# Optimization experiments

Hardware: AMD Instinct MI355X
Metric: run time of the kernel (lower is better)

Reference implementation:

```python
import jax, jax.numpy as jnp
import numpy as np

B, Hh, Ww, C = 16, 56, 56, 384
HEADS, WS, SHIFT = 12, 7, 3
N = WS * WS            # 49 tokens per window
NW = (Hh // WS) * (Ww // WS)  # 64 windows
HID = int(C * 4.0)
SCALE = (C // HEADS) ** -0.5
EPS = 1e-5


def _relative_position_index():
    coords = np.stack(np.meshgrid(np.arange(WS), np.arange(WS), indexing='ij')).reshape(2, -1)
    rel = (coords[:, :, None] - coords[:, None, :]).transpose(1, 2, 0)  # (N,N,2)
    rel[..., 0] += WS - 1
    rel[..., 1] += WS - 1
    rel[..., 0] *= 2 * WS - 1
    return jnp.asarray(rel.sum(-1))  # (N,N) int

RPI = _relative_position_index()


def _swin_mask():
    img = np.zeros((Hh, Ww), np.float32)
    slices = (slice(0, -WS), slice(-WS, -SHIFT), slice(-SHIFT, None))
    cnt = 0
    for hs in slices:
        for ws in slices:
            img[hs, ws] = cnt
            cnt += 1
    m = img.reshape(Hh // WS, WS, Ww // WS, WS).transpose(0, 2, 1, 3).reshape(-1, N)  # (nW,N)
    am = m[:, None, :] - m[:, :, None]
    return jnp.asarray(np.where(am != 0, -100.0, 0.0).astype(np.float32))  # (nW,N,N)


def setup_inputs() -> dict:
    key = jax.random.key(0)
    ks = jax.random.split(key, 12)
    p = lambda k, shp, s=0.02: (jax.random.normal(k, shp, jnp.float32) * s)
    return {
        'x': jax.random.normal(ks[0], (B, Hh * Ww, C), jnp.float32),
        'mask_matrix': _swin_mask(),
        'norm1_g': jnp.ones((C,), jnp.float32),
        'norm1_b': jnp.zeros((C,), jnp.float32),
        'qkv_w': p(ks[1], (3 * C, C)),
        'qkv_b': jnp.zeros((3 * C,), jnp.float32),
        'rpb_table': p(ks[2], ((2 * WS - 1) * (2 * WS - 1), HEADS)),
        'proj_w': p(ks[3], (C, C)),
        'proj_b': jnp.zeros((C,), jnp.float32),
        'norm2_g': jnp.ones((C,), jnp.float32),
        'norm2_b': jnp.zeros((C,), jnp.float32),
        'fc1_w': p(ks[4], (HID, C)),
        'fc1_b': jnp.zeros((HID,), jnp.float32),
        'fc2_w': p(ks[5], (C, HID)),
        'fc2_b': jnp.zeros((C,), jnp.float32),
    }


def _ln(x, g, b):
    m = jnp.mean(x, -1, keepdims=True)
    v = jnp.mean(jnp.square(x - m), -1, keepdims=True)
    return (x - m) * jax.lax.rsqrt(v + EPS) * g + b


def reference(x, mask_matrix, norm1_g, norm1_b, qkv_w, qkv_b, rpb_table,
              proj_w, proj_b, norm2_g, norm2_b, fc1_w, fc1_b, fc2_w, fc2_b):
    shortcut = x
    h = _ln(x, norm1_g, norm1_b).reshape(B, Hh, Ww, C)
    # cyclic shift (H,W divisible by window -> no pad)
    h = jnp.roll(h, (-SHIFT, -SHIFT), axis=(1, 2))
    # window partition -> (B*nW, N, C)
    win = h.reshape(B, Hh // WS, WS, Ww // WS, WS, C).transpose(0, 1, 3, 2, 4, 5).reshape(-1, N, C)
    B_ = win.shape[0]
    hd = C // HEADS
    qkv = (win @ qkv_w.T + qkv_b).reshape(B_, N, 3, HEADS, hd).transpose(2, 0, 3, 1, 4)
    q, k, v = qkv[0] * SCALE, qkv[1], qkv[2]  # (B_,H,N,hd)
    attn = jnp.einsum('bhnd,bhmd->bhnm', q, k)  # (B_,H,N,N)
    bias = rpb_table[RPI]  # (N,N,heads)
    attn = attn + bias.transpose(2, 0, 1)[None]
    attn = attn.reshape(B, NW, HEADS, N, N) + mask_matrix[None, :, None]
    attn = jax.nn.softmax(attn.reshape(B_, HEADS, N, N), axis=-1)
    out = jnp.einsum('bhnm,bhmd->bhnd', attn, v).transpose(0, 2, 1, 3).reshape(B_, N, C)
    out = out @ proj_w.T + proj_b
    # window reverse + reverse shift
    out = out.reshape(B, Hh // WS, Ww // WS, WS, WS, C).transpose(0, 1, 3, 2, 4, 5).reshape(B, Hh, Ww, C)
    out = jnp.roll(out, (SHIFT, SHIFT), axis=(1, 2)).reshape(B, Hh * Ww, C)
    x = shortcut + out
    h2 = _ln(x, norm2_g, norm2_b)
    h2 = jax.nn.gelu(h2 @ fc1_w.T + fc1_b, approximate=False)  # torch nn.GELU exact
    return x + (h2 @ fc2_w.T + fc2_b)
```

## Files before the change

### kernel.cpp

```cpp
#include <hip/hip_runtime.h>

typedef unsigned short u16;
typedef unsigned int u32;
typedef short s16x8 __attribute__((ext_vector_type(8)));
typedef unsigned short u16x4 __attribute__((ext_vector_type(4)));
typedef float f32x4 __attribute__((ext_vector_type(4)));

#define ATTN_SCALE 0.17677669529663687f

__device__ __forceinline__ u16 f2bf(float f) {
  union { float f; u32 i; } c; c.f = f;
  u32 r = c.i + 0x7fffu + ((c.i >> 16) & 1u);
  return (u16)(r >> 16);
}
__device__ __forceinline__ float bf2f(u16 u) {
  union { u32 i; float f; } c; c.i = ((u32)u) << 16; return c.f;
}
__device__ __forceinline__ f32x4 mfma16(s16x8 a, s16x8 b, f32x4 c) {
  return __builtin_amdgcn_mfma_f32_16x16x32_bf16(a, b, c, 0, 0, 0);
}

typedef __attribute__((address_space(1))) u32 gas_u32;
typedef __attribute__((address_space(3))) u32 las_u32;
#define GLL16(gp, lp) __builtin_amdgcn_global_load_lds((gas_u32*)(gp), (las_u32*)(lp), 16, 0, 0)

__device__ __forceinline__ int win_to_orig(int m) {
  int b = m / 3136, rem = m - b * 3136;
  int w = rem / 49, n = rem - w * 49;
  int wh = w >> 3, ww = w & 7;
  int i = n / 7, j = n - i * 7;
  int r = wh * 7 + i + 3; if (r >= 56) r -= 56;
  int c = ww * 7 + j + 3; if (c >= 56) c -= 56;
  return b * 3136 + r * 56 + c;
}

__global__ __launch_bounds__(256) void cvt_all_kernel(
    const float* __restrict__ qkvw, const float* __restrict__ projw,
    const float* __restrict__ fc1w, const float* __restrict__ fc2w,
    u16* __restrict__ wq, u16* __restrict__ wp,
    u16* __restrict__ w1, u16* __restrict__ w2) {
  int i = blockIdx.x * 256 + threadIdx.x;
  if (i < 442368) wq[i] = f2bf(qkvw[i]);
  else if (i < 589824) wp[i - 442368] = f2bf(projw[i - 442368]);
  else if (i < 1179648) w1[i - 589824] = f2bf(fc1w[i - 589824]);
  else if (i < 1769472) w2[i - 1179648] = f2bf(fc2w[i - 1179648]);
}

__global__ __launch_bounds__(256) void mk_tbl_kernel(
    const float* __restrict__ rpb, const float* __restrict__ maskp,
    u16* __restrict__ tbl) {
  int idx = blockIdx.x * 256 + threadIdx.x;
  int wh = idx >> 12;
  int rem = idx & 4095;
  int irow = rem >> 6;
  int lr = (rem >> 2) & 15, ni = rem & 3;
  int j = ni * 16 + lr;
  int wi = wh / 12, h = wh - wi * 12;
  float val = -1e30f;
  if (irow < 49 && j < 49) {
    int yi = irow / 7, xi = irow - yi * 7;
    int yj = j / 7, xj = j - yj * 7;
    int rpi = (yi - yj + 6) * 13 + (xi - xj + 6);
    val = rpb[rpi * 12 + h] + maskp[((size_t)wi * 49 + irow) * 49 + j];
  }
  tbl[idx] = f2bf(val);
}

template <bool PERM, bool BFIN>
__global__ __launch_bounds__(256) void ln_kernel(
    const void* __restrict__ xin, const float* __restrict__ g,
    const float* __restrict__ bb, u16* __restrict__ xo) {
  int t = blockIdx.x * 4 + (threadIdx.x >> 6);
  int l = threadIdx.x & 63;
  int src = PERM ? win_to_orig(t) : t;
  float v[6];
  if (BFIN) {
    const u16* row = (const u16*)xin + (size_t)src * 384;
#pragma unroll
    for (int k = 0; k < 6; k++) v[k] = bf2f(row[l + 64 * k]);
  } else {
    const float* row = (const float*)xin + (size_t)src * 384;
#pragma unroll
    for (int k = 0; k < 6; k++) v[k] = row[l + 64 * k];
  }
  float s = 0.f;
#pragma unroll
  for (int k = 0; k < 6; k++) s += v[k];
#pragma unroll
  for (int d = 1; d < 64; d <<= 1) s += __shfl_xor(s, d);
  float mean = s * (1.f / 384.f);
  float q = 0.f;
#pragma unroll
  for (int k = 0; k < 6; k++) { float dv = v[k] - mean; q += dv * dv; }
#pragma unroll
  for (int d = 1; d < 64; d <<= 1) q += __shfl_xor(q, d);
  float rstd = rsqrtf(q * (1.f / 384.f) + 1e-5f);
  u16* orow = xo + (size_t)t * 384;
#pragma unroll
  for (int k = 0; k < 6; k++) {
    int c = l + 64 * k;
    orow[c] = f2bf((v[k] - mean) * rstd * g[c] + bb[c]);
  }
}

template <int EPI>
__device__ __forceinline__ void gemm_epi(
    float v, size_t m, int col, int N, int dst,
    u16* __restrict__ outb, float* __restrict__ outf,
    const float* __restrict__ auxf, const u16* __restrict__ auxb) {
  if (EPI == 0) {
    outb[m * (size_t)N + col] = f2bf(v);
  } else if (EPI == 1) {
    outb[(size_t)dst * 384 + col] = f2bf(v + auxf[(size_t)dst * 384 + col]);
  } else if (EPI == 2) {
    float u = v * (0.7978845608028654f + 0.0356774081f * v * v);
    float gl = v / (1.f + __expf(-2.f * u));
    outb[m * (size_t)N + col] = f2bf(gl);
  } else {
    outf[m * (size_t)N + col] = v + bf2f(auxb[m * (size_t)N + col]);
  }
}

template <int EPI>
__global__ __launch_bounds__(256) void gemm128_kernel(
    const u16* __restrict__ A, const u16* __restrict__ W,
    const float* __restrict__ bias, u16* __restrict__ outb,
    float* __restrict__ outf, const float* __restrict__ auxf,
    const u16* __restrict__ auxb, int K, int N, int NT, int NB) {
  __shared__ __align__(16) short As[8192];
  __shared__ __align__(16) short Bs[8192];
  const int tid = threadIdx.x, wv = tid >> 6, l = tid & 63;
  const int lr = l & 15, lg = l >> 4;
  int bm, bn;
  {
    const int STS = NT << 3;
    const int body = (NB >> 3) * STS;
    int d = blockIdx.x;
    if (d < body) {
      int st = d / STS, rem = d - st * STS;
      bn = rem >> 3;
      bm = st * 8 + (rem & 7);
    } else {
      int t = d - body;
      int tq = t / NT;
      bm = (NB & ~7) + tq;
      bn = t - tq * NT;
    }
  }
  const size_t m0 = (size_t)bm * 128, n0 = (size_t)bn * 128;
  const int prow = wv * 16 + (l >> 2);
  const int ccl = (((l & 3) ^ ((l >> 3) & 3)) << 3);
  const u16* ga0 = A + (m0 + prow) * K + ccl;
  const u16* ga1 = A + (m0 + 64 + prow) * K + ccl;
  const u16* gb0 = W + (n0 + prow) * K + ccl;
  const u16* gb1 = W + (n0 + 64 + prow) * K + ccl;
  const int stoff = wv * 512;
  const int wr = wv >> 1, wc = wv & 1;
  const int sw = (lr >> 1) & 3;
  const int aoff = (wr * 64 + lr) * 32 + ((lg ^ sw) << 3);
  const int boff = (wc * 64 + lr) * 32 + ((lg ^ sw) << 3);

#define STAGE(bufo, koff)                            \
  do {                                               \
    GLL16(ga0 + (koff), As + (bufo) + stoff);        \
    GLL16(ga1 + (koff), As + (bufo) + 2048 + stoff); \
    GLL16(gb0 + (koff), Bs + (bufo) + stoff);        \
    GLL16(gb1 + (koff), Bs + (bufo) + 2048 + stoff); \
  } while (0)
#define FRAG_READS(cur)                                              \
  do {                                                               \
    const short* as = As + (cur);                                    \
    const short* bs = Bs + (cur);                                    \
    _Pragma("unroll") for (int mi = 0; mi < 4; mi++)                 \
        af[mi] = *(const s16x8*)&as[aoff + mi * 512];                \
    _Pragma("unroll") for (int ni = 0; ni < 4; ni++)                 \
        bfr[ni] = *(const s16x8*)&bs[boff + ni * 512];               \
  } while (0)
#define MFMA_TILE()                                        \
  do {                                                     \
    _Pragma("unroll") for (int mi = 0; mi < 4; mi++)       \
        _Pragma("unroll") for (int ni = 0; ni < 4; ni++)   \
            acc[mi][ni] = mfma16(af[mi], bfr[ni], acc[mi][ni]); \
  } while (0)

  f32x4 acc[4][4] = {};
  s16x8 af[4], bfr[4];
  STAGE(0, 0);
  STAGE(4096, 32);
  int cur = 0;
  int k0 = 0;
  for (; k0 < K - 32; k0 += 32) {
    asm volatile("s_waitcnt vmcnt(4)" ::: "memory");
    __builtin_amdgcn_sched_barrier(0);
    __builtin_amdgcn_s_barrier();
    FRAG_READS(cur);
    asm volatile("s_waitcnt lgkmcnt(0)" ::: "memory");
    __builtin_amdgcn_sched_barrier(0);
    __builtin_amdgcn_s_barrier();
    if (k0 + 64 < K) STAGE(cur, k0 + 64);
    MFMA_TILE();
    cur ^= 4096;
  }
  asm volatile("s_waitcnt vmcnt(0)" ::: "memory");
  __builtin_amdgcn_sched_barrier(0);
  __builtin_amdgcn_s_barrier();
  FRAG_READS(cur);
  asm volatile("s_waitcnt lgkmcnt(0)" ::: "memory");
  __builtin_amdgcn_sched_barrier(0);
  MFMA_TILE();
#undef STAGE
#undef FRAG_READS
#undef MFMA_TILE

  const int colb = (int)n0 + wc * 64;
#pragma unroll
  for (int mi = 0; mi < 4; mi++) {
#pragma unroll
    for (int r = 0; r < 4; r++) {
      const size_t m = m0 + wr * 64 + mi * 16 + lg * 4 + r;
      int dst = 0;
      if (EPI == 1) dst = win_to_orig((int)m);
#pragma unroll
      for (int ni = 0; ni < 4; ni++) {
        const int col = colb + ni * 16 + lr;
        gemm_epi<EPI>(acc[mi][ni][r] + bias[col], m, col, N, dst,
                      outb, outf, auxf, auxb);
      }
    }
  }
}

template <int EPI>
__global__ __launch_bounds__(512) void gemm256_kernel(
    const u16* __restrict__ A, const u16* __restrict__ W,
    const float* __restrict__ bias, u16* __restrict__ outb,
    float* __restrict__ outf, const float* __restrict__ auxf,
    const u16* __restrict__ auxb, int K, int N, int NT, int NB) {
  __shared__ __align__(16) short As[16384];
  __shared__ __align__(16) short Bs[8192];
  const int tid = threadIdx.x, wv = tid >> 6, l = tid & 63;
  const int lr = l & 15, lg = l >> 4;
  int bm, bn;
  {
    const int STS = NT << 3;
    const int body = (NB >> 3) * STS;
    int d = blockIdx.x;
    if (d < body) {
      int st = d / STS, rem = d - st * STS;
      bn = rem >> 3;
      bm = st * 8 + (rem & 7);
    } else {
      int t = d - body;
      int tq = t / NT;
      bm = (NB & ~7) + tq;
      bn = t - tq * NT;
    }
  }
  const size_t m0 = (size_t)bm * 256, n0 = (size_t)bn * 128;
  const int prow = wv * 16 + (l >> 2);
  const int ccl = (((l & 3) ^ ((l >> 3) & 3)) << 3);
  const u16* ga0 = A + (m0 + prow) * K + ccl;
  const u16* ga1 = A + (m0 + 128 + prow) * K + ccl;
  const u16* gb0 = W + (n0 + prow) * K + ccl;
  const int stoff = wv * 512;
  const int wr = wv >> 2, wc = wv & 3;
  const int sw = (lr >> 1) & 3;
  const int aoff = (wr * 128 + lr) * 32 + ((lg ^ sw) << 3);
  const int boff = (wc * 32 + lr) * 32 + ((lg ^ sw) << 3);

#define STAGE(c, koff)                                     \
  do {                                                     \
    GLL16(ga0 + (koff), As + (c) * 8192 + stoff);          \
    GLL16(ga1 + (koff), As + (c) * 8192 + 4096 + stoff);   \
    GLL16(gb0 + (koff), Bs + (c) * 4096 + stoff);          \
  } while (0)
#define FRAG_READS(c)                                                \
  do {                                                               \
    const short* as = As + (c) * 8192;                               \
    const short* bs = Bs + (c) * 4096;                               \
    _Pragma("unroll") for (int mi = 0; mi < 8; mi++)                 \
        af[mi] = *(const s16x8*)&as[aoff + mi * 512];                \
    _Pragma("unroll") for (int ni = 0; ni < 2; ni++)                 \
        bfr[ni] = *(const s16x8*)&bs[boff + ni * 512];               \
  } while (0)
#define MFMA_TILE()                                        \
  do {                                                     \
    __builtin_amdgcn_s_setprio(1);                         \
    _Pragma("unroll") for (int mi = 0; mi < 8; mi++)       \
        _Pragma("unroll") for (int ni = 0; ni < 2; ni++)   \
            acc[mi][ni] = mfma16(af[mi], bfr[ni], acc[mi][ni]); \
    __builtin_amdgcn_s_setprio(0);                         \
  } while (0)

  f32x4 acc[8][2] = {};
  s16x8 af[8], bfr[2];
  STAGE(0, 0);
  STAGE(1, 32);
  int cur = 0;
  int k0 = 0;
  for (; k0 < K - 32; k0 += 32) {
    asm volatile("s_waitcnt vmcnt(3)" ::: "memory");
    __builtin_amdgcn_sched_barrier(0);
    __builtin_amdgcn_s_barrier();
    FRAG_READS(cur);
    asm volatile("s_waitcnt lgkmcnt(0)" ::: "memory");
    __builtin_amdgcn_sched_barrier(0);
    __builtin_amdgcn_s_barrier();
    if (k0 + 64 < K) STAGE(cur, k0 + 64);
    MFMA_TILE();
    cur ^= 1;
  }
  asm volatile("s_waitcnt vmcnt(0)" ::: "memory");
  __builtin_amdgcn_sched_barrier(0);
  __builtin_amdgcn_s_barrier();
  FRAG_READS(cur);
  asm volatile("s_waitcnt lgkmcnt(0)" ::: "memory");
  __builtin_amdgcn_sched_barrier(0);
  MFMA_TILE();
#undef STAGE
#undef FRAG_READS
#undef MFMA_TILE

  const int colb = (int)n0 + wc * 32;
#pragma unroll
  for (int mi = 0; mi < 8; mi++) {
#pragma unroll
    for (int r = 0; r < 4; r++) {
      const size_t m = m0 + wr * 128 + mi * 16 + lg * 4 + r;
      int dst = 0;
      if (EPI == 1) dst = win_to_orig((int)m);
#pragma unroll
      for (int ni = 0; ni < 2; ni++) {
        const int col = colb + ni * 16 + lr;
        gemm_epi<EPI>(acc[mi][ni][r] + bias[col], m, col, N, dst,
                      outb, outf, auxf, auxb);
      }
    }
  }
}

__global__ __launch_bounds__(256) void attn_kernel(
    const u16* __restrict__ qkv, const u16* __restrict__ tbl,
    u16* __restrict__ out) {
  __shared__ __align__(16) short Pl[4][16 * 76];
  const int tid = threadIdx.x, wv = tid >> 6, l = tid & 63;
  const int lr = l & 15, lg = l >> 4;

  const int task = blockIdx.x * 4 + wv;
  const int win = task / 12, h = task - win * 12;
  const int wi = win & 63;
  const short* base = (const short*)qkv + (size_t)win * 49 * 1152 + h * 32;
  const u16* tb = tbl + (size_t)(wi * 12 + h) * 4096 + lr * 4;

  s16x8 qf[4], kf[4];
  const s16x8 zz = {0, 0, 0, 0, 0, 0, 0, 0};
#pragma unroll
  for (int mi = 0; mi < 4; mi++) {
    int n = mi * 16 + lr;
    if (n < 49) {
      qf[mi] = *(const s16x8*)(base + (size_t)n * 1152 + lg * 8);
      kf[mi] = *(const s16x8*)(base + (size_t)n * 1152 + 384 + lg * 8);
    } else { qf[mi] = zz; kf[mi] = zz; }
  }
  s16x8 vb[2][2];
#pragma unroll
  for (int kk = 0; kk < 2; kk++)
#pragma unroll
    for (int nd = 0; nd < 2; nd++)
#pragma unroll
      for (int e = 0; e < 8; e++)
        vb[kk][nd][e] = base[(size_t)(kk * 32 + lg * 8 + e) * 1152 + 768 + nd * 16 + lr];
  u16x4 t4[4][4];
#pragma unroll
  for (int r = 0; r < 4; r++)
    t4[0][r] = *(const u16x4*)&tb[(lg * 4 + r) * 64];

  f32x4 acc[4][4] = {};
  __builtin_amdgcn_s_setprio(1);
#pragma unroll
  for (int mi = 0; mi < 4; mi++)
#pragma unroll
    for (int ni = 0; ni < 4; ni++)
      acc[mi][ni] = mfma16(qf[mi], kf[ni], acc[mi][ni]);
  __builtin_amdgcn_s_setprio(0);

  short* pl = Pl[wv];
#pragma unroll
  for (int mi = 0; mi < 4; mi++) {
    if (mi < 3) {
#pragma unroll
      for (int r = 0; r < 4; r++)
        t4[mi + 1][r] = *(const u16x4*)&tb[((mi + 1) * 16 + lg * 4 + r) * 64];
    }
    float rs[4];
#pragma unroll
    for (int r = 0; r < 4; r++) {
      float sv[4];
#pragma unroll
      for (int ni = 0; ni < 4; ni++)
        sv[ni] = acc[mi][ni][r] * ATTN_SCALE + bf2f(t4[mi][r][ni]);
      float mx = fmaxf(fmaxf(sv[0], sv[1]), fmaxf(sv[2], sv[3]));
#pragma unroll
      for (int d = 1; d < 16; d <<= 1) mx = fmaxf(mx, __shfl_xor(mx, d));
      float sm = 0.f;
#pragma unroll
      for (int ni = 0; ni < 4; ni++) { sv[ni] = __expf(sv[ni] - mx); sm += sv[ni]; }
#pragma unroll
      for (int d = 1; d < 16; d <<= 1) sm += __shfl_xor(sm, d);
      rs[r] = 1.f / sm;
#pragma unroll
      for (int ni = 0; ni < 4; ni++)
        pl[(lg * 4 + r) * 76 + ni * 16 + lr] = (short)f2bf(sv[ni]);
    }
    f32x4 o[2] = {{}, {}};
    __builtin_amdgcn_s_setprio(1);
#pragma unroll
    for (int kk = 0; kk < 2; kk++) {
      s16x8 pa = *(const s16x8*)&pl[lr * 76 + kk * 32 + lg * 8];
#pragma unroll
      for (int nd = 0; nd < 2; nd++)
        o[nd] = mfma16(pa, vb[kk][nd], o[nd]);
    }
    __builtin_amdgcn_s_setprio(0);
#pragma unroll
    for (int r = 0; r < 4; r++) {
      const int irow = mi * 16 + lg * 4 + r;
      if (irow < 49) {
#pragma unroll
        for (int nd = 0; nd < 2; nd++)
          out[((size_t)win * 49 + irow) * 384 + h * 32 + nd * 16 + lr] =
              f2bf(o[nd][r] * rs[r]);
      }
    }
  }
}

extern "C" void kernel_launch(void* const* d_in, const int* in_sizes, int n_in,
                              void* d_out, int out_size, void* d_ws, size_t ws_size,
                              hipStream_t stream) {
  (void)in_sizes; (void)n_in; (void)out_size; (void)ws_size;
  const float* x     = (const float*)d_in[0];
  const float* maskp = (const float*)d_in[1];
  const float* n1g   = (const float*)d_in[2];
  const float* n1b   = (const float*)d_in[3];
  const float* qkvw  = (const float*)d_in[4];
  const float* qkvb  = (const float*)d_in[5];
  const float* rpb   = (const float*)d_in[6];
  const float* projw = (const float*)d_in[7];
  const float* projb = (const float*)d_in[8];
  const float* n2g   = (const float*)d_in[9];
  const float* n2b   = (const float*)d_in[10];
  const float* fc1w  = (const float*)d_in[11];
  const float* fc1b  = (const float*)d_in[12];
  const float* fc2w  = (const float*)d_in[13];
  const float* fc2b  = (const float*)d_in[14];
  float* outp = (float*)d_out;

  char* ws = (char*)d_ws;
  u16*  regA  = (u16*)ws;
  u16*  regB  = (u16*)(ws + 154140672ull);
  u16*  tbl   = (u16*)(ws + 192675840ull);
  u16*  xresb = (u16*)(ws + 192675840ull);
  u16*  wq = (u16*)(ws + 231211008ull);
  u16*  wp = wq + 442368;
  u16*  w1 = wp + 147456;
  u16*  w2 = w1 + 589824;

  cvt_all_kernel<<<6912, 256, 0, stream>>>(qkvw, projw, fc1w, fc2w, wq, wp, w1, w2);
  mk_tbl_kernel<<<12288, 256, 0, stream>>>(rpb, maskp, tbl);
  ln_kernel<true, false><<<12544, 256, 0, stream>>>(x, n1g, n1b, regB);
  gemm256_kernel<0><<<196 * 9, 512, 0, stream>>>(regB, wq, qkvb, regA, nullptr,
                                                 nullptr, nullptr, 384, 1152, 9, 196);
  attn_kernel<<<3072, 256, 0, stream>>>(regA, tbl, regB);
  gemm128_kernel<1><<<392 * 3, 256, 0, stream>>>(regB, wp, projb, xresb, nullptr,
                                                 x, nullptr, 384, 384, 3, 392);
  ln_kernel<false, true><<<12544, 256, 0, stream>>>(xresb, n2g, n2b, regB);
  gemm256_kernel<2><<<196 * 12, 512, 0, stream>>>(regB, w1, fc1b, regA, nullptr,
                                                  nullptr, nullptr, 384, 1536, 12, 196);
  gemm128_kernel<3><<<392 * 3, 256, 0, stream>>>(regA, w2, fc2b, nullptr, outp,
                                                 nullptr, xresb, 1536, 384, 3, 392);
}
```

Measured before the change: 406.6 us.

## Triple-buffer GEMM LDS stages to drop one barrier per k-step

Both GEMM kernels move from a double-buffered LDS pipeline to a triple-buffered ring. With the extra buffer, the next global->LDS prefetch can be issued right after the single barrier without waiting for the fragment reads, which removes the second s_barrier and lgkmcnt wait per iteration. The 128 kernel also gains s_setprio around its MFMA block. The cost is more LDS per block: 48KB for gemm128 and 72KB for gemm256, which may lower occupancy.

```diff
diff --git a/kernel.cpp b/kernel.cpp
--- a/kernel.cpp
+++ b/kernel.cpp
@@ -127,8 +127,8 @@
     const float* __restrict__ bias, u16* __restrict__ outb,
     float* __restrict__ outf, const float* __restrict__ auxf,
     const u16* __restrict__ auxb, int K, int N, int NT, int NB) {
-  __shared__ __align__(16) short As[8192];
-  __shared__ __align__(16) short Bs[8192];
+  __shared__ __align__(16) short As[12288];
+  __shared__ __align__(16) short Bs[12288];
   const int tid = threadIdx.x, wv = tid >> 6, l = tid & 63;
   const int lr = l & 15, lg = l >> 4;
   int bm, bn;
@@ -160,17 +160,17 @@
   const int aoff = (wr * 64 + lr) * 32 + ((lg ^ sw) << 3);
   const int boff = (wc * 64 + lr) * 32 + ((lg ^ sw) << 3);
 
-#define STAGE(bufo, koff)                            \
-  do {                                               \
-    GLL16(ga0 + (koff), As + (bufo) + stoff);        \
-    GLL16(ga1 + (koff), As + (bufo) + 2048 + stoff); \
-    GLL16(gb0 + (koff), Bs + (bufo) + stoff);        \
-    GLL16(gb1 + (koff), Bs + (bufo) + 2048 + stoff); \
-  } while (0)
-#define FRAG_READS(cur)                                              \
+#define STAGE(b, koff)                                     \
+  do {                                                     \
+    GLL16(ga0 + (koff), As + (b) * 4096 + stoff);          \
+    GLL16(ga1 + (koff), As + (b) * 4096 + 2048 + stoff);   \
+    GLL16(gb0 + (koff), Bs + (b) * 4096 + stoff);          \
+    GLL16(gb1 + (koff), Bs + (b) * 4096 + 2048 + stoff);   \
+  } while (0)
+#define FRAG_READS(b)                                                \
   do {                                                               \
-    const short* as = As + (cur);                                    \
-    const short* bs = Bs + (cur);                                    \
+    const short* as = As + (b) * 4096;                               \
+    const short* bs = Bs + (b) * 4096;                               \
     _Pragma("unroll") for (int mi = 0; mi < 4; mi++)                 \
         af[mi] = *(const s16x8*)&as[aoff + mi * 512];                \
     _Pragma("unroll") for (int ni = 0; ni < 4; ni++)                 \
@@ -178,36 +178,29 @@
   } while (0)
 #define MFMA_TILE()                                        \
   do {                                                     \
+    __builtin_amdgcn_s_setprio(1);                         \
     _Pragma("unroll") for (int mi = 0; mi < 4; mi++)       \
         _Pragma("unroll") for (int ni = 0; ni < 4; ni++)   \
             acc[mi][ni] = mfma16(af[mi], bfr[ni], acc[mi][ni]); \
+    __builtin_amdgcn_s_setprio(0);                         \
   } while (0)
 
   f32x4 acc[4][4] = {};
   s16x8 af[4], bfr[4];
+  const int nt = K >> 5;
+  int b0 = 0, b1 = 1, b2 = 2;
   STAGE(0, 0);
-  STAGE(4096, 32);
-  int cur = 0;
-  int k0 = 0;
-  for (; k0 < K - 32; k0 += 32) {
-    asm volatile("s_waitcnt vmcnt(4)" ::: "memory");
+  STAGE(1, 32);
+  for (int t = 0; t < nt; ++t) {
+    if (t + 1 < nt) { asm volatile("s_waitcnt vmcnt(4)" ::: "memory"); }
+    else            { asm volatile("s_waitcnt vmcnt(0)" ::: "memory"); }
     __builtin_amdgcn_sched_barrier(0);
     __builtin_amdgcn_s_barrier();
-    FRAG_READS(cur);
-    asm volatile("s_waitcnt lgkmcnt(0)" ::: "memory");
-    __builtin_amdgcn_sched_barrier(0);
-    __builtin_amdgcn_s_barrier();
-    if (k0 + 64 < K) STAGE(cur, k0 + 64);
+    if (t + 2 < nt) STAGE(b2, (t + 2) * 32);
+    FRAG_READS(b0);
     MFMA_TILE();
-    cur ^= 4096;
-  }
-  asm volatile("s_waitcnt vmcnt(0)" ::: "memory");
-  __builtin_amdgcn_sched_barrier(0);
-  __builtin_amdgcn_s_barrier();
-  FRAG_READS(cur);
-  asm volatile("s_waitcnt lgkmcnt(0)" ::: "memory");
-  __builtin_amdgcn_sched_barrier(0);
-  MFMA_TILE();
+    int tmp = b0; b0 = b1; b1 = b2; b2 = tmp;
+  }
 #undef STAGE
 #undef FRAG_READS
 #undef MFMA_TILE
@@ -236,8 +229,8 @@
     const float* __restrict__ bias, u16* __restrict__ outb,
     float* __restrict__ outf, const float* __restrict__ auxf,
     const u16* __restrict__ auxb, int K, int N, int NT, int NB) {
-  __shared__ __align__(16) short As[16384];
-  __shared__ __align__(16) short Bs[8192];
+  __shared__ __align__(16) short As[24576];
+  __shared__ __align__(16) short Bs[12288];
   const int tid = threadIdx.x, wv = tid >> 6, l = tid & 63;
   const int lr = l & 15, lg = l >> 4;
   int bm, bn;
@@ -268,16 +261,16 @@
   const int aoff = (wr * 128 + lr) * 32 + ((lg ^ sw) << 3);
   const int boff = (wc * 32 + lr) * 32 + ((lg ^ sw) << 3);
 
-#define STAGE(c, koff)                                     \
+#define STAGE(b, koff)                                     \
   do {                                                     \
-    GLL16(ga0 + (koff), As + (c) * 8192 + stoff);          \
-    GLL16(ga1 + (koff), As + (c) * 8192 + 4096 + stoff);   \
-    GLL16(gb0 + (koff), Bs + (c) * 4096 + stoff);          \
-  } while (0)
-#define FRAG_READS(c)                                                \
+    GLL16(ga0 + (koff), As + (b) * 8192 + stoff);          \
+    GLL16(ga1 + (koff), As + (b) * 8192 + 4096 + stoff);   \
+    GLL16(gb0 + (koff), Bs + (b) * 4096 + stoff);          \
+  } while (0)
+#define FRAG_READS(b)                                                \
   do {                                                               \
-    const short* as = As + (c) * 8192;                               \
-    const short* bs = Bs + (c) * 4096;                               \
+    const short* as = As + (b) * 8192;                               \
+    const short* bs = Bs + (b) * 4096;                               \
     _Pragma("unroll") for (int mi = 0; mi < 8; mi++)                 \
         af[mi] = *(const s16x8*)&as[aoff + mi * 512];                \
     _Pragma("unroll") for (int ni = 0; ni < 2; ni++)                 \
@@ -294,29 +287,20 @@
 
   f32x4 acc[8][2] = {};
   s16x8 af[8], bfr[2];
+  const int nt = K >> 5;
+  int b0 = 0, b1 = 1, b2 = 2;
   STAGE(0, 0);
   STAGE(1, 32);
-  int cur = 0;
-  int k0 = 0;
-  for (; k0 < K - 32; k0 += 32) {
-    asm volatile("s_waitcnt vmcnt(3)" ::: "memory");
+  for (int t = 0; t < nt; ++t) {
+    if (t + 1 < nt) { asm volatile("s_waitcnt vmcnt(3)" ::: "memory"); }
+    else            { asm volatile("s_waitcnt vmcnt(0)" ::: "memory"); }
     __builtin_amdgcn_sched_barrier(0);
     __builtin_amdgcn_s_barrier();
-    FRAG_READS(cur);
-    asm volatile("s_waitcnt lgkmcnt(0)" ::: "memory");
-    __builtin_amdgcn_sched_barrier(0);
-    __builtin_amdgcn_s_barrier();
-    if (k0 + 64 < K) STAGE(cur, k0 + 64);
+    if (t + 2 < nt) STAGE(b2, (t + 2) * 32);
+    FRAG_READS(b0);
     MFMA_TILE();
-    cur ^= 1;
-  }
-  asm volatile("s_waitcnt vmcnt(0)" ::: "memory");
-  __builtin_amdgcn_sched_barrier(0);
-  __builtin_amdgcn_s_barrier();
-  FRAG_READS(cur);
-  asm volatile("s_waitcnt lgkmcnt(0)" ::: "memory");
-  __builtin_amdgcn_sched_barrier(0);
-  MFMA_TILE();
+    int tmp = b0; b0 = b1; b1 = b2; b2 = tmp;
+  }
 #undef STAGE
 #undef FRAG_READS
 #undef MFMA_TILE
```

Result: slower. 455.1 us (+11.9%).

## Fuse fc1, GELU and fc2 into a single MLP kernel

Applied to the files above, without the earlier changes.

Replaces the separate fc1+GELU GEMM and the fc2+residual GEMM with one kernel. Each 512-thread block owns 128 rows. It streams 64-column chunks of fc1 and the matching fc2 slices into swizzled LDS, computes the GELU activations into a per-wave LDS scratch, and accumulates the fc2 output in registers. This avoids writing and re-reading the large bf16 hidden activation and shrinks the workspace layout. In exchange, every block reloads the full weights. Each wave handles only 16 rows, so B-fragment reuse from LDS is low, and weight staging is not overlapped with compute. With 392 large-LDS blocks there is also a risk of poor occupancy and tail imbalance.

```diff
diff --git a/kernel.cpp b/kernel.cpp
--- a/kernel.cpp
+++ b/kernel.cpp
@@ -112,12 +112,6 @@
     outb[m * (size_t)N + col] = f2bf(v);
   } else if (EPI == 1) {
     outb[(size_t)dst * 384 + col] = f2bf(v + auxf[(size_t)dst * 384 + col]);
-  } else if (EPI == 2) {
-    float u = v * (0.7978845608028654f + 0.0356774081f * v * v);
-    float gl = v / (1.f + __expf(-2.f * u));
-    outb[m * (size_t)N + col] = f2bf(gl);
-  } else {
-    outf[m * (size_t)N + col] = v + bf2f(auxb[m * (size_t)N + col]);
   }
 }
 
@@ -339,6 +333,95 @@
   }
 }
 
+__global__ __launch_bounds__(512, 2) void mlp_kernel(
+    const u16* __restrict__ xln, const u16* __restrict__ w1,
+    const float* __restrict__ b1, const u16* __restrict__ w2,
+    const float* __restrict__ b2, const u16* __restrict__ xres,
+    float* __restrict__ out) {
+  __shared__ __align__(16) short W1s[24576];
+  __shared__ __align__(16) short W2s[24576];
+  __shared__ __align__(16) short Ps[8][16 * 136];
+  const int tid = threadIdx.x, wv = tid >> 6, l = tid & 63;
+  const int lr = l & 15, lg = l >> 4;
+  const size_t m0 = (size_t)blockIdx.x * 128;
+  const int arow = (int)m0 + wv * 16 + lr;
+
+  s16x8 a12[12];
+#pragma unroll
+  for (int kk = 0; kk < 12; kk++)
+    a12[kk] = *(const s16x8*)(xln + (size_t)arow * 384 + kk * 32 + lg * 8);
+
+  const int si = tid * 6;
+  f32x4 oacc[24] = {};
+  short* ps = Ps[wv];
+
+  for (int c = 0; c < 24; ++c) {
+#pragma unroll
+    for (int i = 0; i < 6; i++) {
+      int idx = si + i;
+      int r1 = idx / 48, c1 = idx - r1 * 48;
+      s16x8 v1 = *(const s16x8*)(w1 + (size_t)(c * 64 + r1) * 384 + c1 * 8);
+      *(s16x8*)((char*)W1s + (((r1 * 768 + c1 * 16)) ^ ((r1 & 7) << 4))) = v1;
+      int r2 = idx >> 3, c2 = idx & 7;
+      s16x8 v2 = *(const s16x8*)(w2 + (size_t)r2 * 1536 + c * 64 + c2 * 8);
+      *(s16x8*)((char*)W2s + (((r2 * 128 + c2 * 16)) ^ ((r2 & 7) << 4))) = v2;
+    }
+    __syncthreads();
+
+    f32x4 pacc[4] = {};
+    __builtin_amdgcn_s_setprio(1);
+#pragma unroll
+    for (int kk = 0; kk < 12; kk++) {
+#pragma unroll
+      for (int n = 0; n < 4; n++) {
+        const int row = n * 16 + lr;
+        s16x8 bf = *(const s16x8*)((char*)W1s +
+            ((row * 768 + kk * 64 + lg * 16) ^ ((row & 7) << 4)));
+        pacc[n] = mfma16(a12[kk], bf, pacc[n]);
+      }
+    }
+    __builtin_amdgcn_s_setprio(0);
+
+#pragma unroll
+    for (int n = 0; n < 4; n++) {
+      const float bv = b1[c * 64 + n * 16 + lr];
+#pragma unroll
+      for (int r = 0; r < 4; r++) {
+        float v = pacc[n][r] + bv;
+        float u = v * (0.7978845608028654f + 0.0356774081f * v * v);
+        float gl = v / (1.f + __expf(-2.f * u));
+        ps[(lg * 4 + r) * 136 + n * 16 + lr] = (short)f2bf(gl);
+      }
+    }
+
+    __builtin_amdgcn_s_setprio(1);
+#pragma unroll
+    for (int kk = 0; kk < 2; kk++) {
+      s16x8 pa = *(const s16x8*)&ps[lr * 136 + kk * 32 + lg * 8];
+#pragma unroll
+      for (int n2 = 0; n2 < 24; n2++) {
+        const int row = n2 * 16 + lr;
+        s16x8 bf = *(const s16x8*)((char*)W2s +
+            ((row * 128 + kk * 64 + lg * 16) ^ ((row & 7) << 4)));
+        oacc[n2] = mfma16(pa, bf, oacc[n2]);
+      }
+    }
+    __builtin_amdgcn_s_setprio(0);
+    __syncthreads();
+  }
+
+#pragma unroll
+  for (int n2 = 0; n2 < 24; n2++) {
+    const int col = n2 * 16 + lr;
+    const float bv = b2[col];
+#pragma unroll
+    for (int r = 0; r < 4; r++) {
+      const size_t m = m0 + wv * 16 + lg * 4 + r;
+      out[m * 384 + col] = oacc[n2][r] + bv + bf2f(xres[m * 384 + col]);
+    }
+  }
+}
+
 __global__ __launch_bounds__(256) void attn_kernel(
     const u16* __restrict__ qkv, const u16* __restrict__ tbl,
     u16* __restrict__ out) {
@@ -458,10 +541,10 @@
 
   char* ws = (char*)d_ws;
   u16*  regA  = (u16*)ws;
-  u16*  regB  = (u16*)(ws + 154140672ull);
-  u16*  tbl   = (u16*)(ws + 192675840ull);
-  u16*  xresb = (u16*)(ws + 192675840ull);
-  u16*  wq = (u16*)(ws + 231211008ull);
+  u16*  regB  = (u16*)(ws + 115605504ull);
+  u16*  tbl   = (u16*)(ws + 154140672ull);
+  u16*  xresb = (u16*)(ws + 154140672ull);
+  u16*  wq = (u16*)(ws + 192675840ull);
   u16*  wp = wq + 442368;
   u16*  w1 = wp + 147456;
   u16*  w2 = w1 + 589824;
@@ -475,8 +558,5 @@
   gemm128_kernel<1><<<392 * 3, 256, 0, stream>>>(regB, wp, projb, xresb, nullptr,
                                                  x, nullptr, 384, 384, 3, 392);
   ln_kernel<false, true><<<12544, 256, 0, stream>>>(xresb, n2g, n2b, regB);
-  gemm256_kernel<2><<<196 * 12, 512, 0, stream>>>(regB, w1, fc1b, regA, nullptr,
-                                                  nullptr, nullptr, 384, 1536, 12, 196);
-  gemm128_kernel<3><<<392 * 3, 256, 0, stream>>>(regA, w2, fc2b, nullptr, outp,
-                                                 nullptr, xresb, 1536, 384, 3, 392);
-}
+  mlp_kernel<<<392, 512, 0, stream>>>(regB, w1, fc1b, w2, fc2b, xresb, outp);
+}
```

Measured after the change: 834.9 us. +105.3%, slower.
